# Performance work log

Measured on AMD Instinct MI355X. Metric: run time of the kernel, lower is better.

## Reference

```python
import jax, jax.numpy as jnp
import numpy as np

B, N, C, MODES, L = 32, 4096, 128, 32, 4
KIN, KMODES = 256, 64
OUT = C * C * MODES  # outsize = size_in*size_in*modes


def setup_inputs() -> dict:
    key = jax.random.key(0)
    ks = jax.random.split(key, 16)
    sN = lambda k, shape, sc: jax.random.normal(k, shape, jnp.float32) * sc
    inp = {
        "x": jax.random.normal(ks[0], (B, N, 3), jnp.float32),
        "y": jax.random.normal(ks[1], (B, KIN), jnp.float32),
        # fc0: Linear(3 -> C)
        "fc0_w": sN(ks[2], (3, C), 0.5),
        "fc0_b": jnp.zeros((C,), jnp.float32),
        # KernelNetwork (green): y -> [B, C, C, MODES] spectral weights, per layer
        "g1_w": sN(ks[3], (L, KIN, KMODES), 1.0 / np.sqrt(KIN)),
        "g1_b": jnp.zeros((L, KMODES), jnp.float32),
        "g2_w": sN(ks[4], (L, KMODES, OUT), 1.0 / (np.sqrt(KMODES) * C)),
        "g2_b": jnp.zeros((L, OUT), jnp.float32),
        # LinearKernelNetwork: y -> [B, C, C] per-sample mixing matrix, per layer
        "l1_w": sN(ks[5], (L, KIN, KMODES), 1.0 / np.sqrt(KIN)),
        "l1_b": jnp.zeros((L, KMODES), jnp.float32),
        "l2_w": sN(ks[6], (L, KMODES, C * C), 1.0 / (np.sqrt(KMODES) * C)),
        "l2_b": jnp.zeros((L, C * C), jnp.float32),
        # fc1: Linear(C -> 128), fc2: Linear(128 -> 1)
        "fc1_w": sN(ks[7], (C, 128), 1.0 / np.sqrt(C)),
        "fc1_b": jnp.zeros((128,), jnp.float32),
        "fc2_w": sN(ks[8], (128, 1), 1.0 / np.sqrt(128)),
        "fc2_b": jnp.zeros((1,), jnp.float32),
        "weightx": jax.random.uniform(ks[9], (1,), jnp.float32),
    }
    return inp


def _gelu(v):
    return jax.nn.gelu(v, approximate=False)  # torch default (erf) gelu


def reference(x, y, fc0_w, fc0_b, g1_w, g1_b, g2_w, g2_b,
              l1_w, l1_b, l2_w, l2_b, fc1_w, fc1_b, fc2_w, fc2_b, weightx):
    x = x @ fc0_w + fc0_b            # [B, N, C]
    x = x.transpose(0, 2, 1)         # [B, C, N]
    n = x.shape[-1]
    nf = n // 2 + 1
    for i in range(L):
        # green[i](y): spectral weights per sample
        hg = _gelu(y @ g1_w[i] + g1_b[i])
        w_spec = (hg @ g2_w[i] + g2_b[i]).reshape(B, C, C, MODES)
        # FourierKernel: rfft -> multiply low modes with per-sample weights -> irfft
        xft = jnp.fft.rfft(x, axis=-1)                      # [B, C, nf] complex
        om = jnp.einsum('bim,biom->bom', xft[..., :MODES],
                        w_spec.astype(jnp.complex64))        # [B, C, MODES]
        out_ft = jnp.pad(om, ((0, 0), (0, 0), (0, nf - MODES)))
        x1 = jnp.fft.irfft(out_ft, n=n, axis=-1)             # [B, C, N]
        # lin_layer_real[i](y) + batch_conv_1d == per-sample CxC matmul
        hl = _gelu(y @ l1_w[i] + l1_b[i])
        w_lin = (hl @ l2_w[i] + l2_b[i]).reshape(B, C, C)
        x2 = jnp.einsum('boi,bin->bon', w_lin, x)            # [B, C, N]
        x = x1 + x2
        if i < L - 1:
            x = _gelu(x)
    x = x.transpose(0, 2, 1)          # [B, N, C]
    x = _gelu(x @ fc1_w + fc1_b)
    x = x @ fc2_w + fc2_b             # [B, N, 1]
    return x * weightx
```

## Files before the change

kernel.cpp:

```cpp
#include <hip/hip_runtime.h>

typedef _Float16 half_t;
typedef _Float16 f16x8 __attribute__((ext_vector_type(8)));
typedef float    f32x4 __attribute__((ext_vector_type(4)));

#define MFMA16(a, b, c) __builtin_amdgcn_mfma_f32_16x16x32_f16((a), (b), (c), 0, 0, 0)

struct __align__(4) h2 { half_t a, b; };

__device__ __forceinline__ float gelu_f(float v) {
    return 0.5f * v * (1.0f + erff(v * 0.70710678118654752440f));
}

__global__ __launch_bounds__(256) void prep(half_t* __restrict__ TT, half_t* __restrict__ ITT,
                                            half_t* __restrict__ FC1WT, const float* __restrict__ fc1w) {
    int id = blockIdx.x * 256 + threadIdx.x;
    if (id < 262144) {
        int c = id >> 12, n = id & 4095;
        int m = c & 31;
        int ph = (m * n) & 4095;
        float ang = (float)ph * (6.283185307179586f / 4096.0f);
        float cv = cosf(ang), sv = sinf(ang);
        TT[(size_t)c * 4096 + n] = (half_t)((c < 32) ? cv : -sv);
        ITT[(size_t)n * 64 + c]  = (half_t)((c < 32) ? cv : sv);
    } else if (id < 262144 + 16384) {
        int p = id - 262144;
        int j = p >> 7, c = p & 127;
        FC1WT[j * 128 + c] = (half_t)fc1w[c * 128 + j];
    }
}

__global__ __launch_bounds__(64) void knet1(const float* __restrict__ y,
                                            const float* __restrict__ g1w, const float* __restrict__ g1b,
                                            const float* __restrict__ l1w, const float* __restrict__ l1b,
                                            float* __restrict__ HGt, float* __restrict__ HLt) {
    int bid = blockIdx.x;
    int which = bid & 1, b = (bid >> 1) & 31, l = bid >> 6;
    int kp = threadIdx.x;
    const float* w  = (which ? l1w : g1w) + (size_t)l * 256 * 64;
    const float* bb = (which ? l1b : g1b) + l * 64;
    const float* yb = y + b * 256;
    float acc = bb[kp];
    for (int k = 0; k < 256; ++k) acc += yb[k] * w[(size_t)k * 64 + kp];
    float g = gelu_f(acc);
    (which ? HLt : HGt)[((size_t)l * 64 + kp) * 32 + b] = g;
}

__global__ __launch_bounds__(128) void knet2(const float* __restrict__ HLt, const float* __restrict__ l2w,
                                             const float* __restrict__ l2b, half_t* __restrict__ WLIN) {
    int l = blockIdx.x >> 7, o = blockIdx.x & 127, i = threadIdx.x;
    float acc[32];
    float bias = l2b[(size_t)l * 16384 + o * 128 + i];
#pragma unroll
    for (int b = 0; b < 32; ++b) acc[b] = bias;
    const float* w = l2w + (size_t)l * 64 * 16384 + o * 128 + i;
    const float* h = HLt + l * 2048;
#pragma unroll 4
    for (int k = 0; k < 64; ++k) {
        float wv = w[(size_t)k * 16384];
        const float* hr = h + k * 32;
#pragma unroll
        for (int b = 0; b < 32; ++b) acc[b] += hr[b] * wv;
    }
#pragma unroll
    for (int b = 0; b < 32; ++b)
        WLIN[(((size_t)l * 32 + b) * 128 + o) * 128 + i] = (half_t)acc[b];
}

__global__ __launch_bounds__(256) void fc0k(const float* __restrict__ xin, const float* __restrict__ w,
                                            const float* __restrict__ bias,
                                            half_t* __restrict__ XN, half_t* __restrict__ XT) {
    __shared__ float lx[384];
    int b = blockIdx.x >> 5, nt = blockIdx.x & 31;
    int n0 = nt * 128;
    for (int t = threadIdx.x; t < 384; t += 256) lx[t] = xin[((size_t)b * 4096 + n0) * 3 + t];
    __syncthreads();
#pragma unroll 4
    for (int rr = 0; rr < 32; ++rr) {
        int p = threadIdx.x + rr * 256;
        int c = p >> 6, n2 = (p & 63) * 2;
        float v0 = bias[c] + lx[n2 * 3] * w[c] + lx[n2 * 3 + 1] * w[128 + c] + lx[n2 * 3 + 2] * w[256 + c];
        int n3 = n2 + 1;
        float v1 = bias[c] + lx[n3 * 3] * w[c] + lx[n3 * 3 + 1] * w[128 + c] + lx[n3 * 3 + 2] * w[256 + c];
        h2 hv; hv.a = (half_t)v0; hv.b = (half_t)v1;
        *(h2*)(XN + ((size_t)b * 128 + c) * 4096 + n0 + n2) = hv;
    }
#pragma unroll 4
    for (int rr = 0; rr < 32; ++rr) {
        int p = threadIdx.x + rr * 256;
        int n = p >> 6, c2 = (p & 63) * 2;
        float v0 = bias[c2]     + lx[n * 3] * w[c2]     + lx[n * 3 + 1] * w[128 + c2]     + lx[n * 3 + 2] * w[256 + c2];
        float v1 = bias[c2 + 1] + lx[n * 3] * w[c2 + 1] + lx[n * 3 + 1] * w[128 + c2 + 1] + lx[n * 3 + 2] * w[256 + c2 + 1];
        h2 hv; hv.a = (half_t)v0; hv.b = (half_t)v1;
        *(h2*)(XT + ((size_t)b * 4096 + n0 + n) * 128 + c2) = hv;
    }
}

__global__ __launch_bounds__(256) void fwd_dft(const half_t* __restrict__ XN, const half_t* __restrict__ TT,
                                               float* __restrict__ XFTP) {
    int tile = blockIdx.x, ks = blockIdx.y;
    int wave = threadIdx.x >> 6, lane = threadIdx.x & 63;
    int lm = lane & 15, lq = lane >> 4;
    int r0 = tile * 64 + wave * 16;
    int kbase = ks * 512;
    f32x4 acc[4];
#pragma unroll
    for (int ct = 0; ct < 4; ++ct) acc[ct] = (f32x4){0.f, 0.f, 0.f, 0.f};
    const half_t* arow = XN + (size_t)(r0 + lm) * 4096 + kbase + lq * 8;
#pragma unroll 4
    for (int kk = 0; kk < 16; ++kk) {
        f16x8 a = *(const f16x8*)(arow + kk * 32);
#pragma unroll
        for (int ct = 0; ct < 4; ++ct) {
            const half_t* bp = TT + (size_t)(ct * 16 + lm) * 4096 + kbase + kk * 32 + lq * 8;
            f16x8 bf = *(const f16x8*)bp;
            acc[ct] = MFMA16(a, bf, acc[ct]);
        }
    }
    float* outp = XFTP + (size_t)ks * 262144;
#pragma unroll
    for (int ct = 0; ct < 4; ++ct)
#pragma unroll
        for (int r = 0; r < 4; ++r) {
            int row = r0 + lq * 4 + r;
            outp[(size_t)row * 64 + ct * 16 + lm] = acc[ct][r];
        }
}

__global__ __launch_bounds__(256) void red_xft(const float* __restrict__ XFTP, float* __restrict__ XFT) {
    int i = blockIdx.x * 256 + threadIdx.x;
    float s = 0.f;
#pragma unroll
    for (int p = 0; p < 8; ++p) s += XFTP[(size_t)p * 262144 + i];
    XFT[i] = s;
}

__global__ __launch_bounds__(256) void spec_w(const float* __restrict__ hg, const float* __restrict__ g2w_l,
                                              const float* __restrict__ g2b_l, half_t* __restrict__ WSPEC) {
    int jg = threadIdx.x & 63;
    int bg = __builtin_amdgcn_readfirstlane((int)(threadIdx.x >> 6));
    int b0 = bg * 8;
    size_t jbase = (size_t)blockIdx.x * 512 + jg * 8;
    float acc[8][8];
#pragma unroll
    for (int i = 0; i < 8; ++i)
#pragma unroll
        for (int q = 0; q < 8; ++q) acc[i][q] = 0.f;
#pragma unroll 4
    for (int k = 0; k < 64; ++k) {
        const float* wr = g2w_l + (size_t)k * 524288 + jbase;
        float4 w0 = *(const float4*)wr;
        float4 w1 = *(const float4*)(wr + 4);
        const float* hr = hg + k * 32 + b0;
#pragma unroll
        for (int bb = 0; bb < 8; ++bb) {
            float h = hr[bb];
            acc[bb][0] += h * w0.x; acc[bb][1] += h * w0.y;
            acc[bb][2] += h * w0.z; acc[bb][3] += h * w0.w;
            acc[bb][4] += h * w1.x; acc[bb][5] += h * w1.y;
            acc[bb][6] += h * w1.z; acc[bb][7] += h * w1.w;
        }
    }
    float4 bv0 = *(const float4*)(g2b_l + jbase);
    float4 bv1 = *(const float4*)(g2b_l + jbase + 4);
    float bvs[8] = {bv0.x, bv0.y, bv0.z, bv0.w, bv1.x, bv1.y, bv1.z, bv1.w};
#pragma unroll
    for (int bb = 0; bb < 8; ++bb) {
        f16x8 hv;
#pragma unroll
        for (int q = 0; q < 8; ++q) hv[q] = (half_t)(acc[bb][q] + bvs[q]);
        *(f16x8*)(WSPEC + (size_t)(b0 + bb) * 524288 + jbase) = hv;
    }
}

__global__ __launch_bounds__(256) void om_k(const half_t* __restrict__ WSPEC, const float* __restrict__ XFT,
                                            half_t* __restrict__ OMC) {
    __shared__ float xs[128 * 64];
    int b = blockIdx.x >> 4, ob = blockIdx.x & 15;
    for (int t = threadIdx.x; t < 8192; t += 256) xs[t] = XFT[(size_t)b * 8192 + t];
    __syncthreads();
    int o = ob * 8 + (threadIdx.x >> 5), m = threadIdx.x & 31;
    const half_t* wp = WSPEC + (size_t)b * 524288 + o * 32 + m;
    float re = 0.f, im = 0.f;
#pragma unroll 8
    for (int i = 0; i < 128; ++i) {
        float w = (float)wp[(size_t)i * 4096];
        re += w * xs[i * 64 + m];
        im += w * xs[i * 64 + 32 + m];
    }
    float cm = (m == 0) ? (1.0f / 4096.0f) : (2.0f / 4096.0f);
    OMC[((size_t)b * 128 + o) * 64 + m]      = (half_t)(re * cm);
    OMC[((size_t)b * 128 + o) * 64 + 32 + m] = (half_t)(-im * cm);
}

__global__ __launch_bounds__(256) void layer_out(const half_t* __restrict__ ITT, const half_t* __restrict__ OMC,
                                                 const half_t* __restrict__ WLIN_l,
                                                 half_t* __restrict__ XT, half_t* __restrict__ XN,
                                                 float inv_s, float sout, int do_gelu, int do_xn) {
    __shared__ half_t ts[64 * 130];
    int b = blockIdx.x >> 6, ntile = blockIdx.x & 63;
    int wave = threadIdx.x >> 6, lane = threadIdx.x & 63;
    int lm = lane & 15, lq = lane >> 4;
    int n0w = ntile * 64 + wave * 16;
    f32x4 acc[8];
#pragma unroll
    for (int ot = 0; ot < 8; ++ot) acc[ot] = (f32x4){0.f, 0.f, 0.f, 0.f};

    const half_t* arow1 = ITT + (size_t)(n0w + lm) * 64 + lq * 8;
    const half_t* brow1 = OMC + ((size_t)b * 128 + lm) * 64 + lq * 8;
#pragma unroll
    for (int kk = 0; kk < 2; ++kk) {
        f16x8 a = *(const f16x8*)(arow1 + kk * 32);
#pragma unroll
        for (int ot = 0; ot < 8; ++ot) {
            f16x8 bf = *(const f16x8*)(brow1 + (size_t)ot * 1024 + kk * 32);
            acc[ot] = MFMA16(a, bf, acc[ot]);
        }
    }
    const half_t* arow2 = XT + ((size_t)b * 4096 + n0w + lm) * 128 + lq * 8;
    const half_t* brow2 = WLIN_l + ((size_t)b * 128 + lm) * 128 + lq * 8;
#pragma unroll
    for (int kk = 0; kk < 4; ++kk) {
        f16x8 a = *(const f16x8*)(arow2 + kk * 32);
#pragma unroll
        for (int ot = 0; ot < 8; ++ot) {
            f16x8 bf = *(const f16x8*)(brow2 + (size_t)ot * 2048 + kk * 32);
            acc[ot] = MFMA16(a, bf, acc[ot]);
        }
    }
#pragma unroll
    for (int ot = 0; ot < 8; ++ot) {
        int o = ot * 16 + lm;
#pragma unroll
        for (int r = 0; r < 4; ++r) {
            int n = wave * 16 + lq * 4 + r;
            float v = acc[ot][r] * inv_s;
            if (do_gelu) v = gelu_f(v);
            ts[n * 130 + o] = (half_t)(v * sout);
        }
    }
    __syncthreads();
#pragma unroll 4
    for (int rr = 0; rr < 16; ++rr) {
        int p = threadIdx.x + rr * 256;
        int n = p >> 6, oc = p & 63;
        uint32_t v = *(const uint32_t*)(ts + n * 130 + 2 * oc);
        *(uint32_t*)(XT + ((size_t)b * 4096 + ntile * 64 + n) * 128 + 2 * oc) = v;
    }
    if (do_xn) {
        int np = threadIdx.x & 31, o8 = threadIdx.x >> 5;
#pragma unroll 4
        for (int rr = 0; rr < 16; ++rr) {
            int o = o8 + 8 * rr;
            int n = 2 * np;
            h2 hv; hv.a = ts[n * 130 + o]; hv.b = ts[(n + 1) * 130 + o];
            *(h2*)(XN + ((size_t)b * 128 + o) * 4096 + ntile * 64 + n) = hv;
        }
    }
}

__global__ __launch_bounds__(256) void head(const half_t* __restrict__ XT, const half_t* __restrict__ FC1WT,
                                            const float* __restrict__ fc1b, const float* __restrict__ fc2w,
                                            const float* __restrict__ fc2bias, const float* __restrict__ wx,
                                            float* __restrict__ out, float inv_s) {
    int tile = blockIdx.x;
    int wave = threadIdx.x >> 6, lane = threadIdx.x & 63;
    int lm = lane & 15, lq = lane >> 4;
    int r0 = tile * 64 + wave * 16;
    f32x4 acc[8];
#pragma unroll
    for (int jt = 0; jt < 8; ++jt) acc[jt] = (f32x4){0.f, 0.f, 0.f, 0.f};
    const half_t* arow = XT + (size_t)(r0 + lm) * 128 + lq * 8;
#pragma unroll
    for (int kk = 0; kk < 4; ++kk) {
        f16x8 a = *(const f16x8*)(arow + kk * 32);
#pragma unroll
        for (int jt = 0; jt < 8; ++jt) {
            f16x8 bf = *(const f16x8*)(FC1WT + (size_t)(jt * 16 + lm) * 128 + kk * 32 + lq * 8);
            acc[jt] = MFMA16(a, bf, acc[jt]);
        }
    }
    float sr[4] = {0.f, 0.f, 0.f, 0.f};
#pragma unroll
    for (int jt = 0; jt < 8; ++jt) {
        int j = jt * 16 + lm;
        float b1 = fc1b[j], w2 = fc2w[j];
#pragma unroll
        for (int r = 0; r < 4; ++r) {
            float v = acc[jt][r] * inv_s + b1;
            v = gelu_f(v);
            sr[r] += v * w2;
        }
    }
#pragma unroll
    for (int r = 0; r < 4; ++r) {
        float s = sr[r];
        s += __shfl_xor(s, 1);
        s += __shfl_xor(s, 2);
        s += __shfl_xor(s, 4);
        s += __shfl_xor(s, 8);
        if (lm == 0) {
            int row = r0 + lq * 4 + r;
            out[row] = (s + fc2bias[0]) * wx[0];
        }
    }
}

extern "C" void kernel_launch(void* const* d_in, const int* in_sizes, int n_in,
                              void* d_out, int out_size, void* d_ws, size_t ws_size,
                              hipStream_t stream) {
    const float* x_in = (const float*)d_in[0];
    const float* y    = (const float*)d_in[1];
    const float* fc0w = (const float*)d_in[2];
    const float* fc0b = (const float*)d_in[3];
    const float* g1w  = (const float*)d_in[4];
    const float* g1b  = (const float*)d_in[5];
    const float* g2w  = (const float*)d_in[6];
    const float* g2b  = (const float*)d_in[7];
    const float* l1w  = (const float*)d_in[8];
    const float* l1b  = (const float*)d_in[9];
    const float* l2w  = (const float*)d_in[10];
    const float* l2b  = (const float*)d_in[11];
    const float* fc1w = (const float*)d_in[12];
    const float* fc1b = (const float*)d_in[13];
    const float* fc2w = (const float*)d_in[14];
    const float* fc2b = (const float*)d_in[15];
    const float* wx   = (const float*)d_in[16];
    float* out = (float*)d_out;

    char* p = (char*)d_ws;
    half_t* XT    = (half_t*)p; p += 33554432;
    half_t* XN    = (half_t*)p; p += 33554432;
    half_t* WSPEC = (half_t*)p; p += 33554432;
    half_t* TT    = (half_t*)p; p += 524288;
    half_t* ITT   = (half_t*)p; p += 524288;
    half_t* FC1WT = (half_t*)p; p += 32768;
    float*  HGt   = (float*)p;  p += 32768;
    float*  HLt   = (float*)p;  p += 32768;
    half_t* WLIN  = (half_t*)p; p += 4194304;
    float*  XFTP  = (float*)p;  p += 8388608;
    float*  XFT   = (float*)p;  p += 1048576;
    half_t* OMC   = (half_t*)p; p += 524288;

    prep<<<1088, 256, 0, stream>>>(TT, ITT, FC1WT, fc1w);
    knet1<<<256, 64, 0, stream>>>(y, g1w, g1b, l1w, l1b, HGt, HLt);
    knet2<<<512, 128, 0, stream>>>(HLt, l2w, l2b, WLIN);
    fc0k<<<1024, 256, 0, stream>>>(x_in, fc0w, fc0b, XN, XT);

    const float S[5] = {1.f, 16.f, 256.f, 4096.f, 65536.f};
    for (int l = 0; l < 4; ++l) {
        fwd_dft<<<dim3(64, 8), 256, 0, stream>>>(XN, TT, XFTP);
        red_xft<<<1024, 256, 0, stream>>>(XFTP, XFT);
        spec_w<<<1024, 256, 0, stream>>>(HGt + l * 2048, g2w + (size_t)l * 64 * 524288,
                                         g2b + (size_t)l * 524288, WSPEC);
        om_k<<<512, 256, 0, stream>>>(WSPEC, XFT, OMC);
        layer_out<<<2048, 256, 0, stream>>>(ITT, OMC, WLIN + (size_t)l * 524288, XT, XN,
                                            1.0f / S[l], S[l + 1], (l < 3) ? 1 : 0, (l < 3) ? 1 : 0);
    }
    head<<<2048, 256, 0, stream>>>(XT, FC1WT, fc1b, fc2w, fc2b, wx, out, 1.0f / S[4]);
}
```

Measured before the change: 1.262 ms.

## Fuse split-K DFT reduction into om_k, reshape DFT blocks, nontemporal spec_w loads

The separate red_xft reduction kernel is removed. om_k now sums the eight split-K partials of XFTP directly into shared memory, and each thread computes two modes using packed half loads. fwd_dft runs with 128-thread blocks over twice as many tiles, and spec_w streams the large g2 weight tensor with nontemporal loads. The aim is to save a launch and one round trip of the XFT buffer through memory, and to keep the streamed weights from polluting the cache. In exchange, every om_k block re-reads the partials for its batch: 16 blocks per batch each re-sum the same 8x data.

```diff
diff --git a/kernel.cpp b/kernel.cpp
--- a/kernel.cpp
+++ b/kernel.cpp
@@ -96,12 +96,12 @@
     }
 }
 
-__global__ __launch_bounds__(256) void fwd_dft(const half_t* __restrict__ XN, const half_t* __restrict__ TT,
+__global__ __launch_bounds__(128) void fwd_dft(const half_t* __restrict__ XN, const half_t* __restrict__ TT,
                                                float* __restrict__ XFTP) {
     int tile = blockIdx.x, ks = blockIdx.y;
     int wave = threadIdx.x >> 6, lane = threadIdx.x & 63;
     int lm = lane & 15, lq = lane >> 4;
-    int r0 = tile * 64 + wave * 16;
+    int r0 = tile * 32 + wave * 16;
     int kbase = ks * 512;
     f32x4 acc[4];
 #pragma unroll
@@ -125,14 +125,6 @@
             int row = r0 + lq * 4 + r;
             outp[(size_t)row * 64 + ct * 16 + lm] = acc[ct][r];
         }
-}
-
-__global__ __launch_bounds__(256) void red_xft(const float* __restrict__ XFTP, float* __restrict__ XFT) {
-    int i = blockIdx.x * 256 + threadIdx.x;
-    float s = 0.f;
-#pragma unroll
-    for (int p = 0; p < 8; ++p) s += XFTP[(size_t)p * 262144 + i];
-    XFT[i] = s;
 }
 
 __global__ __launch_bounds__(256) void spec_w(const float* __restrict__ hg, const float* __restrict__ g2w_l,
@@ -148,22 +140,22 @@
         for (int q = 0; q < 8; ++q) acc[i][q] = 0.f;
 #pragma unroll 4
     for (int k = 0; k < 64; ++k) {
-        const float* wr = g2w_l + (size_t)k * 524288 + jbase;
-        float4 w0 = *(const float4*)wr;
-        float4 w1 = *(const float4*)(wr + 4);
+        const f32x4* wr = (const f32x4*)(g2w_l + (size_t)k * 524288 + jbase);
+        f32x4 w0 = __builtin_nontemporal_load(wr);
+        f32x4 w1 = __builtin_nontemporal_load(wr + 1);
         const float* hr = hg + k * 32 + b0;
 #pragma unroll
         for (int bb = 0; bb < 8; ++bb) {
             float h = hr[bb];
-            acc[bb][0] += h * w0.x; acc[bb][1] += h * w0.y;
-            acc[bb][2] += h * w0.z; acc[bb][3] += h * w0.w;
-            acc[bb][4] += h * w1.x; acc[bb][5] += h * w1.y;
-            acc[bb][6] += h * w1.z; acc[bb][7] += h * w1.w;
-        }
-    }
-    float4 bv0 = *(const float4*)(g2b_l + jbase);
-    float4 bv1 = *(const float4*)(g2b_l + jbase + 4);
-    float bvs[8] = {bv0.x, bv0.y, bv0.z, bv0.w, bv1.x, bv1.y, bv1.z, bv1.w};
+            acc[bb][0] += h * w0[0]; acc[bb][1] += h * w0[1];
+            acc[bb][2] += h * w0[2]; acc[bb][3] += h * w0[3];
+            acc[bb][4] += h * w1[0]; acc[bb][5] += h * w1[1];
+            acc[bb][6] += h * w1[2]; acc[bb][7] += h * w1[3];
+        }
+    }
+    f32x4 bv0 = *(const f32x4*)(g2b_l + jbase);
+    f32x4 bv1 = *(const f32x4*)(g2b_l + jbase + 4);
+    float bvs[8] = {bv0[0], bv0[1], bv0[2], bv0[3], bv1[0], bv1[1], bv1[2], bv1[3]};
 #pragma unroll
     for (int bb = 0; bb < 8; ++bb) {
         f16x8 hv;
@@ -173,24 +165,41 @@
     }
 }
 
-__global__ __launch_bounds__(256) void om_k(const half_t* __restrict__ WSPEC, const float* __restrict__ XFT,
+__global__ __launch_bounds__(128) void om_k(const half_t* __restrict__ WSPEC, const float* __restrict__ XFTP,
                                             half_t* __restrict__ OMC) {
-    __shared__ float xs[128 * 64];
+    __shared__ float xs[8192];
     int b = blockIdx.x >> 4, ob = blockIdx.x & 15;
-    for (int t = threadIdx.x; t < 8192; t += 256) xs[t] = XFT[(size_t)b * 8192 + t];
+    for (int t = threadIdx.x; t < 2048; t += 128) {
+        const float* base = XFTP + (size_t)b * 8192 + t * 4;
+        f32x4 s = {0.f, 0.f, 0.f, 0.f};
+#pragma unroll
+        for (int p = 0; p < 8; ++p) {
+            f32x4 v = *(const f32x4*)(base + (size_t)p * 262144);
+            s += v;
+        }
+        *(f32x4*)(xs + t * 4) = s;
+    }
     __syncthreads();
-    int o = ob * 8 + (threadIdx.x >> 5), m = threadIdx.x & 31;
-    const half_t* wp = WSPEC + (size_t)b * 524288 + o * 32 + m;
-    float re = 0.f, im = 0.f;
+    int o = ob * 8 + (threadIdx.x >> 4);
+    int m2 = (threadIdx.x & 15) * 2;
+    const half_t* wp = WSPEC + (size_t)b * 524288 + o * 32 + m2;
+    float re0 = 0.f, im0 = 0.f, re1 = 0.f, im1 = 0.f;
 #pragma unroll 8
     for (int i = 0; i < 128; ++i) {
-        float w = (float)wp[(size_t)i * 4096];
-        re += w * xs[i * 64 + m];
-        im += w * xs[i * 64 + 32 + m];
-    }
-    float cm = (m == 0) ? (1.0f / 4096.0f) : (2.0f / 4096.0f);
-    OMC[((size_t)b * 128 + o) * 64 + m]      = (half_t)(re * cm);
-    OMC[((size_t)b * 128 + o) * 64 + 32 + m] = (half_t)(-im * cm);
+        h2 w = *(const h2*)(wp + (size_t)i * 4096);
+        float w0 = (float)w.a, w1 = (float)w.b;
+        float2 xr = *(const float2*)(xs + i * 64 + m2);
+        float2 xi = *(const float2*)(xs + i * 64 + 32 + m2);
+        re0 += w0 * xr.x; im0 += w0 * xi.x;
+        re1 += w1 * xr.y; im1 += w1 * xi.y;
+    }
+    float c0 = (m2 == 0) ? (1.0f / 4096.0f) : (2.0f / 4096.0f);
+    float c1 = 2.0f / 4096.0f;
+    size_t obase = ((size_t)b * 128 + o) * 64;
+    h2 hr; hr.a = (half_t)(re0 * c0); hr.b = (half_t)(re1 * c1);
+    h2 hi; hi.a = (half_t)(-im0 * c0); hi.b = (half_t)(-im1 * c1);
+    *(h2*)(OMC + obase + m2) = hr;
+    *(h2*)(OMC + obase + 32 + m2) = hi;
 }
 
 __global__ __launch_bounds__(256) void layer_out(const half_t* __restrict__ ITT, const half_t* __restrict__ OMC,
@@ -339,7 +348,6 @@
     float*  HLt   = (float*)p;  p += 32768;
     half_t* WLIN  = (half_t*)p; p += 4194304;
     float*  XFTP  = (float*)p;  p += 8388608;
-    float*  XFT   = (float*)p;  p += 1048576;
     half_t* OMC   = (half_t*)p; p += 524288;
 
     prep<<<1088, 256, 0, stream>>>(TT, ITT, FC1WT, fc1w);
@@ -349,11 +357,10 @@
 
     const float S[5] = {1.f, 16.f, 256.f, 4096.f, 65536.f};
     for (int l = 0; l < 4; ++l) {
-        fwd_dft<<<dim3(64, 8), 256, 0, stream>>>(XN, TT, XFTP);
-        red_xft<<<1024, 256, 0, stream>>>(XFTP, XFT);
+        fwd_dft<<<dim3(128, 8), 128, 0, stream>>>(XN, TT, XFTP);
         spec_w<<<1024, 256, 0, stream>>>(HGt + l * 2048, g2w + (size_t)l * 64 * 524288,
                                          g2b + (size_t)l * 524288, WSPEC);
-        om_k<<<512, 256, 0, stream>>>(WSPEC, XFT, OMC);
+        om_k<<<512, 128, 0, stream>>>(WSPEC, XFTP, OMC);
         layer_out<<<2048, 256, 0, stream>>>(ITT, OMC, WLIN + (size_t)l * 524288, XT, XN,
                                             1.0f / S[l], S[l + 1], (l < 3) ? 1 : 0, (l < 3) ? 1 : 0);
     }
```

New measurement: 1.388 ms. 10.0% more time.
